# Optimization experiments

Measured on AMD Instinct MI355X. Metric: run time of the kernel, lower is better.

## Reference

```python
import jax, jax.numpy as jnp
import numpy as np
from jax import lax


def conv2d(x, w, b=None, pad=0):
    y = lax.conv_general_dilated(x, w, (1, 1), [(pad, pad), (pad, pad)],
                                 dimension_numbers=('NCHW', 'OIHW', 'NCHW'))
    if b is not None:
        y = y + b[None, :, None, None]
    return y


def setup_inputs():
    key = jax.random.key(0)
    ks = jax.random.split(key, 8)
    B, C, H, W = 8, 3, 224, 224
    OC, NH, HD = 32, 8, 4
    s = lambda fan: 1.0 / np.sqrt(fan)
    x = jax.random.normal(ks[0], (B, C, H, W), jnp.float32)
    # gumbel noise for the hard gumbel-softmax over attention logits [B,NH,HD,H,H]
    gumbel = jax.random.gumbel(ks[1], (B, NH, HD, H, H), jnp.float32)
    in_w = jax.random.normal(ks[2], (OC, C, 3, 3), jnp.float32) * s(C * 9)
    in_b = jnp.zeros((OC,), jnp.float32)
    qkv_w = jax.random.normal(ks[3], (3 * OC, OC, 3, 3), jnp.float32) * s(OC * 9)
    proj_w = jax.random.normal(ks[4], (OC, OC, 1, 1), jnp.float32) * s(OC)
    proj_b = jnp.zeros((OC,), jnp.float32)
    upd_w = jax.random.normal(ks[5], (OC, OC, 1, 1), jnp.float32) * s(OC)
    upd_b = jnp.zeros((OC,), jnp.float32)
    bn_gamma = jnp.ones((OC,), jnp.float32)
    bn_beta = jnp.zeros((OC,), jnp.float32)
    return {"x": x, "gumbel": gumbel, "in_w": in_w, "in_b": in_b, "qkv_w": qkv_w,
            "proj_w": proj_w, "proj_b": proj_b, "upd_w": upd_w, "upd_b": upd_b,
            "bn_gamma": bn_gamma, "bn_beta": bn_beta}


def reference(x, gumbel, in_w, in_b, qkv_w, proj_w, proj_b, upd_w, upd_b, bn_gamma, bn_beta):
    B, _, H, W = x.shape
    NH, HD = 8, 4
    OC = NH * HD
    EPS = 1e-5
    x1 = conv2d(x, in_w, in_b, pad=1)                       # [B,32,H,W]
    qkv = conv2d(x1, qkv_w, None, pad=1).reshape(B, NH, 3, HD, H, W)
    q, k, v = qkv[:, :, 0], qkv[:, :, 1], qkv[:, :, 2]      # each [B,NH,HD,H,W]
    scale = HD ** -0.5
    # matmul(q, k^T) over the last two dims -> [B,NH,HD,H,H]
    logits = jnp.einsum('bndiw,bndjw->bndij', q, k) * scale
    # hard gumbel-softmax, tau=1, straight-through
    y_soft = jax.nn.softmax(logits + gumbel, axis=-1)
    idx = jnp.argmax(y_soft, axis=-1)
    y_hard = jax.nn.one_hot(idx, H, dtype=y_soft.dtype)
    att = y_hard - lax.stop_gradient(y_soft) + y_soft
    A = jnp.einsum('bndij,bndjw->bndiw', att, v).reshape(B, OC, H, W)
    # F.interpolate to (224,224) bilinear is identity since H=W=224
    A = conv2d(A, proj_w, proj_b)
    A = conv2d(A, upd_w, upd_b)
    # BatchNorm2d in training mode (batch statistics, biased variance)
    mean = A.mean(axis=(0, 2, 3), keepdims=True)
    var = ((A - mean) ** 2).mean(axis=(0, 2, 3), keepdims=True)
    A = (A - mean) * lax.rsqrt(var + EPS)
    A = A * bn_gamma[None, :, None, None] + bn_beta[None, :, None, None]
    A = A * jax.nn.sigmoid(A)  # SiLU; dropout is identity (eval)
    out = A + x1
    return out, att
```

## Files before the change

### kernel.cpp

```cpp
#include <hip/hip_runtime.h>
#include <hip/hip_bf16.h>

#define NB 8
#define CIN 3
#define HH 224
#define WW 224
#define OC 32
#define NH 8
#define HD 4
#define NHD 32
#define C96 96
#define HWSZ (HH*WW)

#define HT 4
#define OCT 8
#define NGB 4

__global__ void k_w2(const float* __restrict__ pw, const float* __restrict__ pb,
                     const float* __restrict__ uw, const float* __restrict__ ub,
                     float* __restrict__ W2, float* __restrict__ b2) {
    int c = threadIdx.x, o = threadIdx.y;
    float acc = 0.f;
    for (int m = 0; m < OC; ++m) acc = fmaf(uw[o*OC + m], pw[m*OC + c], acc);
    W2[o*OC + c] = acc;
    if (c == 0) {
        float bb = ub[o];
        for (int m = 0; m < OC; ++m) bb = fmaf(uw[o*OC + m], pb[m], bb);
        b2[o] = bb;
    }
}

__global__ __launch_bounds__(256) void k_conv_in_tile(const float* __restrict__ x,
                                                      const float* __restrict__ w,
                                                      const float* __restrict__ bias,
                                                      float* __restrict__ x1) {
    int h0 = blockIdx.x * 2;
    int b  = blockIdx.y;
    __shared__ float xs[CIN][4][226];
    int t = threadIdx.x;
    for (int ch = 0; ch < CIN; ++ch)
        for (int r = 0; r < 4; ++r) {
            int gh = h0 - 1 + r;
            for (int col = t; col < 226; col += 256) {
                float v = 0.f;
                if (gh >= 0 && gh < HH && col > 0 && col < 225)
                    v = x[((size_t)(b*CIN + ch)*HH + gh)*WW + (col-1)];
                xs[ch][r][col] = v;
            }
        }
    __syncthreads();
    int wv = t;
    if (wv >= WW) return;
    float xv[CIN][4][3];
    #pragma unroll
    for (int c = 0; c < CIN; ++c)
        #pragma unroll
        for (int r = 0; r < 4; ++r)
            #pragma unroll
            for (int j = 0; j < 3; ++j)
                xv[c][r][j] = xs[c][r][wv + j];
    float acc[2][OC];
    #pragma unroll
    for (int hy = 0; hy < 2; ++hy)
        for (int oc = 0; oc < OC; ++oc) acc[hy][oc] = 0.f;
    #pragma unroll
    for (int c = 0; c < CIN; ++c)
        #pragma unroll
        for (int kh = 0; kh < 3; ++kh)
            #pragma unroll
            for (int kw = 0; kw < 3; ++kw)
                for (int oc = 0; oc < OC; ++oc) {
                    float wgt = w[oc*CIN*9 + c*9 + kh*3 + kw];
                    #pragma unroll
                    for (int hy = 0; hy < 2; ++hy)
                        acc[hy][oc] = fmaf(xv[c][hy+kh][kw], wgt, acc[hy][oc]);
                }
    for (int oc = 0; oc < OC; ++oc) {
        float bs = bias[oc];
        #pragma unroll
        for (int hy = 0; hy < 2; ++hy)
            x1[((size_t)(b*OC + oc)*HH + (h0+hy))*WW + wv] = __fadd_rn(acc[hy][oc], bs);
    }
}

__global__ __launch_bounds__(256) void k_conv_qkv_tile(const float* __restrict__ x1g,
                                                       const float* __restrict__ w,
                                                       float* __restrict__ qk4,
                                                       float* __restrict__ vbg) {
    int h0 = blockIdx.x * HT;
    int og = blockIdx.y * OCT;
    int z  = blockIdx.z;
    const float* x1b = x1g + (size_t)z*OC*HWSZ;
    float* qk = qk4 + (size_t)z*64*HWSZ;
    float* vb = vbg + (size_t)z*OC*HWSZ;
    __shared__ float xs[2][HT+2][226];
    int t = threadIdx.x;
    int wv = t;
    float acc[HT][OCT];
    #pragma unroll
    for (int a = 0; a < HT; ++a)
        #pragma unroll
        for (int o = 0; o < OCT; ++o) acc[a][o] = 0.f;

    for (int r = 0; r < HT+2; ++r) {
        int gh = h0 - 1 + r;
        for (int col = t; col < 226; col += 256) {
            float v = 0.f;
            if (gh >= 0 && gh < HH && col > 0 && col < 225)
                v = x1b[((size_t)0*HH + gh)*WW + (col-1)];
            xs[0][r][col] = v;
        }
    }
    __syncthreads();

    for (int c = 0; c < OC; ++c) {
        int cur = c & 1;
        if (c + 1 < OC) {
            int nxt = cur ^ 1;
            for (int r = 0; r < HT+2; ++r) {
                int gh = h0 - 1 + r;
                for (int col = t; col < 226; col += 256) {
                    float v = 0.f;
                    if (gh >= 0 && gh < HH && col > 0 && col < 225)
                        v = x1b[((size_t)(c+1)*HH + gh)*WW + (col-1)];
                    xs[nxt][r][col] = v;
                }
            }
        }
        if (wv < WW) {
            float xv[HT+2][3];
            #pragma unroll
            for (int r = 0; r < HT+2; ++r)
                #pragma unroll
                for (int j = 0; j < 3; ++j)
                    xv[r][j] = xs[cur][r][wv + j];
            #pragma unroll
            for (int o = 0; o < OCT; ++o) {
                const float* wr = w + ((size_t)(og + o)*OC + c)*9;
                #pragma unroll
                for (int kh = 0; kh < 3; ++kh)
                    #pragma unroll
                    for (int kw = 0; kw < 3; ++kw) {
                        float wgt = wr[kh*3 + kw];
                        #pragma unroll
                        for (int hy = 0; hy < HT; ++hy)
                            acc[hy][o] = fmaf(xv[hy+kh][kw], wgt, acc[hy][o]);
                    }
            }
        }
        __syncthreads();
    }
    if (wv < WW) {
        #pragma unroll
        for (int o = 0; o < OCT; ++o) {
            int oc = og + o;
            int n = oc / 12, rem = oc % 12;
            int r = rem >> 2, d = rem & 3;
            #pragma unroll
            for (int hy = 0; hy < HT; ++hy) {
                int h = h0 + hy;
                if (r < 2)
                    qk[((size_t)(n*8 + r*4 + d)*HH + h)*WW + wv] = acc[hy][o];
                else
                    vb[((size_t)(n*4 + d)*HH + h)*WW + wv] = acc[hy][o];
            }
        }
    }
}

__global__ __launch_bounds__(256) void k_attn_ri(const float* __restrict__ qk,
                                                 const float* __restrict__ gum,
                                                 float* __restrict__ att,
                                                 int* __restrict__ idxout) {
    int i0 = blockIdx.x * 8;
    int nd = blockIdx.y;
    int n = nd >> 2, d = nd & 3;
    const float* qb = qk + ((size_t)(n*8 + d)*HH + i0)*WW;
    const float* kb = qk + ((size_t)(n*8 + 4 + d)*HH)*WW;
    __shared__ __align__(16) float qs[8][WW];
    __shared__ float vals[8][256];
    __shared__ int   win_s[8];
    int t = threadIdx.x;
    for (int f = t; f < 8*(WW/4); f += 256) {
        int r = f / (WW/4), p = (f % (WW/4))*4;
        *(float4*)(&qs[r][p]) = *(const float4*)(qb + (size_t)r*WW + p);
    }
    __syncthreads();
    if (t < WW) {
        const float* kr = kb + (size_t)t*WW;
        float s0[8], s1[8], s2[8], s3[8];
        #pragma unroll
        for (int ii = 0; ii < 8; ++ii) { s0[ii]=0.f; s1[ii]=0.f; s2[ii]=0.f; s3[ii]=0.f; }
        for (int w = 0; w < WW; w += 4) {
            float4 kc = *(const float4*)(kr + w);
            #pragma unroll
            for (int ii = 0; ii < 8; ++ii) {
                float4 qc = *(const float4*)(&qs[ii][w]);
                s0[ii] = __fadd_rn(s0[ii], __fmul_rn(qc.x, kc.x));
                s1[ii] = __fadd_rn(s1[ii], __fmul_rn(qc.y, kc.y));
                s2[ii] = __fadd_rn(s2[ii], __fmul_rn(qc.z, kc.z));
                s3[ii] = __fadd_rn(s3[ii], __fmul_rn(qc.w, kc.w));
            }
        }
        #pragma unroll
        for (int ii = 0; ii < 8; ++ii) {
            float dot = __fadd_rn(__fadd_rn(s0[ii], s1[ii]), __fadd_rn(s2[ii], s3[ii]));
            vals[ii][t] = __fadd_rn(__fmul_rn(0.5f, dot),
                                    gum[((size_t)nd*HH + (i0 + ii))*HH + t]);
        }
    } else {
        #pragma unroll
        for (int ii = 0; ii < 8; ++ii) vals[ii][t] = -INFINITY;
    }
    __syncthreads();
    int ii = t >> 5, jj = t & 31;
    float best = -INFINITY; int bj = 0x7fffffff;
    for (int j = jj; j < 256; j += 32) {
        float v = vals[ii][j];
        if (v > best) { best = v; bj = j; }
    }
    for (int off = 16; off > 0; off >>= 1) {
        float v2 = __shfl_down(best, off, 32);
        int   j2 = __shfl_down(bj,   off, 32);
        if (v2 > best || (v2 == best && j2 < bj)) { best = v2; bj = j2; }
    }
    if (jj == 0) { win_s[ii] = bj; idxout[nd*HH + i0 + ii] = bj; }
    __syncthreads();
    for (int e = t; e < 8*WW; e += 256) {
        int r = e / WW, j = e - r*WW;
        att[((size_t)nd*HH + (i0 + r))*HH + j] = (j == win_s[r]) ? 1.f : 0.f;
    }
}

__global__ void k_gather_mm(const float* __restrict__ vbuf,
                            const int* __restrict__ idx,
                            const float* __restrict__ W2g,
                            const float* __restrict__ b2g,
                            float* __restrict__ A2) {
    int i = blockIdx.x, b = blockIdx.y;
    __shared__ float w2s[OC*OC];
    __shared__ float b2s[OC];
    __shared__ int   id[OC];
    for (int t = threadIdx.x; t < OC*OC; t += blockDim.x) w2s[t] = W2g[t];
    if (threadIdx.x < OC) {
        b2s[threadIdx.x] = b2g[threadIdx.x];
        id[threadIdx.x]  = idx[(b*NHD + threadIdx.x)*HH + i];
    }
    __syncthreads();
    int wv = threadIdx.x;
    if (wv >= WW) return;
    float vals[OC];
    for (int c = 0; c < OC; ++c)
        vals[c] = vbuf[((size_t)(b*OC + c)*HH + id[c])*WW + wv];
    for (int oc = 0; oc < OC; ++oc) {
        float a = b2s[oc];
        for (int c = 0; c < OC; ++c) a = fmaf(w2s[oc*OC + c], vals[c], a);
        A2[((size_t)(b*OC + oc)*HH + i)*WW + wv] = a;
    }
}

__global__ __launch_bounds__(256) void k_stats(const float* __restrict__ A2,
                                               float* __restrict__ sums,
                                               float* __restrict__ sumsq) {
    int oc = blockIdx.x, s = blockIdx.y;
    int t = threadIdx.x;
    float a = 0.f, a2 = 0.f;
    const int SL = HWSZ/16;
    for (int b = 0; b < NB; ++b) {
        const float* base = A2 + (size_t)(b*OC + oc)*HWSZ + s*SL;
        for (int e = t*4; e < SL; e += 256*4) {
            float4 v = *(const float4*)(base + e);
            a  += v.x + v.y + v.z + v.w;
            a2 += v.x*v.x + v.y*v.y + v.z*v.z + v.w*v.w;
        }
    }
    __shared__ float r1[256], r2[256];
    r1[t] = a; r2[t] = a2;
    __syncthreads();
    for (int st = 128; st > 0; st >>= 1) {
        if (t < st) { r1[t] += r1[t+st]; r2[t] += r2[t+st]; }
        __syncthreads();
    }
    if (t == 0) { atomicAdd(&sums[oc], r1[0]); atomicAdd(&sumsq[oc], r2[0]); }
}

__global__ __launch_bounds__(256) void k_final(const float* __restrict__ A2,
                                               const float* __restrict__ x1,
                                               const float* __restrict__ sums,
                                               const float* __restrict__ sumsq,
                                               const float* __restrict__ gamma,
                                               const float* __restrict__ beta,
                                               float* __restrict__ out) {
    int i = blockIdx.x, b = blockIdx.y;
    __shared__ float mean_s[OC], inv_s[OC], g_s[OC], be_s[OC];
    if (threadIdx.x < OC) {
        int oc = threadIdx.x;
        const float N = (float)(NB*HH*WW);
        float mean = sums[oc]/N;
        float var  = sumsq[oc]/N - mean*mean;
        mean_s[oc] = mean;
        inv_s[oc]  = rsqrtf(var + 1e-5f);
        g_s[oc]    = gamma[oc];
        be_s[oc]   = beta[oc];
    }
    __syncthreads();
    int wv = threadIdx.x;
    if (wv >= WW) return;
    for (int oc = 0; oc < OC; ++oc) {
        size_t o = ((size_t)(b*OC + oc)*HH + i)*WW + wv;
        float a = A2[o];
        float an = (a - mean_s[oc])*inv_s[oc]*g_s[oc] + be_s[oc];
        float sw = an / (1.f + __expf(-an));
        out[o] = sw + x1[o];
    }
}

extern "C" void kernel_launch(void* const* d_in, const int* in_sizes, int n_in,
                              void* d_out, int out_size, void* d_ws, size_t ws_size,
                              hipStream_t stream) {
    const float* x      = (const float*)d_in[0];
    const float* gumbel = (const float*)d_in[1];
    const float* in_w   = (const float*)d_in[2];
    const float* in_b   = (const float*)d_in[3];
    const float* qkv_w  = (const float*)d_in[4];
    const float* proj_w = (const float*)d_in[5];
    const float* proj_b = (const float*)d_in[6];
    const float* upd_w  = (const float*)d_in[7];
    const float* upd_b  = (const float*)d_in[8];
    const float* bng    = (const float*)d_in[9];
    const float* bnb    = (const float*)d_in[10];

    float* out = (float*)d_out;
    float* att = out + (size_t)NB*OC*HWSZ;

    float* x1   = (float*)d_ws;
    float* qk4  = x1 + (size_t)NB*OC*HWSZ;
    float* A2   = qk4;
    float* vbuf = qk4 + (size_t)NGB*64*HWSZ;
    float* W2   = vbuf + (size_t)NB*OC*HWSZ;
    float* b2   = W2 + OC*OC;
    float* sums = b2 + OC;
    float* sumsq= sums + OC;
    int*   idx  = (int*)(sumsq + OC);

    hipMemsetAsync(sums, 0, 2*OC*sizeof(float), stream);

    k_w2          <<<1, dim3(OC, OC), 0, stream>>>(proj_w, proj_b, upd_w, upd_b, W2, b2);
    k_conv_in_tile<<<dim3(HH/2, NB), 256, 0, stream>>>(x, in_w, in_b, x1);

    for (int g = 0; g < NB/NGB; ++g) {
        k_conv_qkv_tile<<<dim3(HH/HT, C96/OCT, NGB), 256, 0, stream>>>(
            x1 + (size_t)g*NGB*OC*HWSZ, qkv_w, qk4, vbuf + (size_t)g*NGB*OC*HWSZ);
        for (int z = 0; z < NGB; ++z) {
            int b = g*NGB + z;
            k_attn_ri<<<dim3(HH/8, NHD), 256, 0, stream>>>(
                qk4    + (size_t)z*64*HWSZ,
                gumbel + (size_t)b*NH*HD*HH*HH,
                att    + (size_t)b*NH*HD*HH*HH,
                idx    + (size_t)b*NHD*HH);
        }
    }

    k_gather_mm<<<dim3(HH, NB), 256, 0, stream>>>(vbuf, idx, W2, b2, A2);
    k_stats    <<<dim3(OC, 16), 256, 0, stream>>>(A2, sums, sumsq);
    k_final    <<<dim3(HH, NB), 256, 0, stream>>>(A2, x1, sums, sumsq, bng, bnb, out);
}
```

Baseline: 881.8 us.

## Pad x1 buffer for vectorized halo loads, regroup qkv conv per head, batch attention launches

x1 is now stored in a zero-padded 226x228 layout, and a memset clears its border. The qkv conv can then copy halo rows with unguarded float4 loads instead of branchy scalar loads. The conv block now computes all 12 channels of one head (OCT 12), which simplifies the output index math but raises register pressure. The four per-batch attention launches are merged into one launch with a z grid dimension, at the cost of an extra full-buffer memset and a larger workspace.

```diff
diff --git a/kernel.cpp b/kernel.cpp
--- a/kernel.cpp
+++ b/kernel.cpp
@@ -12,8 +12,12 @@
 #define C96 96
 #define HWSZ (HH*WW)
 
+#define PH 226
+#define PW 228
+#define CHS (PH*PW)
+
 #define HT 4
-#define OCT 8
+#define OCT 12
 #define NGB 4
 
 __global__ void k_w2(const float* __restrict__ pw, const float* __restrict__ pb,
@@ -79,7 +83,7 @@
         float bs = bias[oc];
         #pragma unroll
         for (int hy = 0; hy < 2; ++hy)
-            x1[((size_t)(b*OC + oc)*HH + (h0+hy))*WW + wv] = __fadd_rn(acc[hy][oc], bs);
+            x1[((size_t)(b*OC + oc)*PH + (h0+hy+1))*PW + (wv+1)] = __fadd_rn(acc[hy][oc], bs);
     }
 }
 
@@ -88,44 +92,34 @@
                                                        float* __restrict__ qk4,
                                                        float* __restrict__ vbg) {
     int h0 = blockIdx.x * HT;
-    int og = blockIdx.y * OCT;
+    int n  = blockIdx.y;
     int z  = blockIdx.z;
-    const float* x1b = x1g + (size_t)z*OC*HWSZ;
+    const float* x1b = x1g + (size_t)z*OC*CHS;
     float* qk = qk4 + (size_t)z*64*HWSZ;
     float* vb = vbg + (size_t)z*OC*HWSZ;
-    __shared__ float xs[2][HT+2][226];
+    __shared__ float xs[2][(HT+2)*PW];
     int t = threadIdx.x;
     int wv = t;
+    int og = n * OCT;
     float acc[HT][OCT];
     #pragma unroll
     for (int a = 0; a < HT; ++a)
         #pragma unroll
         for (int o = 0; o < OCT; ++o) acc[a][o] = 0.f;
 
-    for (int r = 0; r < HT+2; ++r) {
-        int gh = h0 - 1 + r;
-        for (int col = t; col < 226; col += 256) {
-            float v = 0.f;
-            if (gh >= 0 && gh < HH && col > 0 && col < 225)
-                v = x1b[((size_t)0*HH + gh)*WW + (col-1)];
-            xs[0][r][col] = v;
-        }
+    {
+        const float4* s = (const float4*)(x1b + (size_t)h0*PW);
+        float4* d = (float4*)xs[0];
+        for (int f = t; f < (HT+2)*PW/4; f += 256) d[f] = s[f];
     }
     __syncthreads();
 
     for (int c = 0; c < OC; ++c) {
         int cur = c & 1;
         if (c + 1 < OC) {
-            int nxt = cur ^ 1;
-            for (int r = 0; r < HT+2; ++r) {
-                int gh = h0 - 1 + r;
-                for (int col = t; col < 226; col += 256) {
-                    float v = 0.f;
-                    if (gh >= 0 && gh < HH && col > 0 && col < 225)
-                        v = x1b[((size_t)(c+1)*HH + gh)*WW + (col-1)];
-                    xs[nxt][r][col] = v;
-                }
-            }
+            const float4* s = (const float4*)(x1b + (size_t)(c+1)*CHS + (size_t)h0*PW);
+            float4* d = (float4*)xs[cur ^ 1];
+            for (int f = t; f < (HT+2)*PW/4; f += 256) d[f] = s[f];
         }
         if (wv < WW) {
             float xv[HT+2][3];
@@ -133,7 +127,7 @@
             for (int r = 0; r < HT+2; ++r)
                 #pragma unroll
                 for (int j = 0; j < 3; ++j)
-                    xv[r][j] = xs[cur][r][wv + j];
+                    xv[r][j] = xs[cur][r*PW + wv + j];
             #pragma unroll
             for (int o = 0; o < OCT; ++o) {
                 const float* wr = w + ((size_t)(og + o)*OC + c)*9;
@@ -153,9 +147,7 @@
     if (wv < WW) {
         #pragma unroll
         for (int o = 0; o < OCT; ++o) {
-            int oc = og + o;
-            int n = oc / 12, rem = oc % 12;
-            int r = rem >> 2, d = rem & 3;
+            int r = o >> 2, d = o & 3;
             #pragma unroll
             for (int hy = 0; hy < HT; ++hy) {
                 int h = h0 + hy;
@@ -168,15 +160,22 @@
     }
 }
 
-__global__ __launch_bounds__(256) void k_attn_ri(const float* __restrict__ qk,
+__global__ __launch_bounds__(256) void k_attn_ri(const float* __restrict__ qk4,
                                                  const float* __restrict__ gum,
                                                  float* __restrict__ att,
-                                                 int* __restrict__ idxout) {
+                                                 int* __restrict__ idxout,
+                                                 int b0) {
     int i0 = blockIdx.x * 8;
     int nd = blockIdx.y;
+    int z  = blockIdx.z;
+    int b  = b0 + z;
+    const float* qkz = qk4 + (size_t)z*64*HWSZ;
+    const float* gumb = gum + (size_t)b*NHD*HH*HH;
+    float* attb = att + (size_t)b*NHD*HH*HH;
+    int* idxb = idxout + (size_t)b*NHD*HH;
     int n = nd >> 2, d = nd & 3;
-    const float* qb = qk + ((size_t)(n*8 + d)*HH + i0)*WW;
-    const float* kb = qk + ((size_t)(n*8 + 4 + d)*HH)*WW;
+    const float* qb = qkz + ((size_t)(n*8 + d)*HH + i0)*WW;
+    const float* kb = qkz + ((size_t)(n*8 + 4 + d)*HH)*WW;
     __shared__ __align__(16) float qs[8][WW];
     __shared__ float vals[8][256];
     __shared__ int   win_s[8];
@@ -206,7 +205,7 @@
         for (int ii = 0; ii < 8; ++ii) {
             float dot = __fadd_rn(__fadd_rn(s0[ii], s1[ii]), __fadd_rn(s2[ii], s3[ii]));
             vals[ii][t] = __fadd_rn(__fmul_rn(0.5f, dot),
-                                    gum[((size_t)nd*HH + (i0 + ii))*HH + t]);
+                                    gumb[((size_t)nd*HH + (i0 + ii))*HH + t]);
         }
     } else {
         #pragma unroll
@@ -224,11 +223,11 @@
         int   j2 = __shfl_down(bj,   off, 32);
         if (v2 > best || (v2 == best && j2 < bj)) { best = v2; bj = j2; }
     }
-    if (jj == 0) { win_s[ii] = bj; idxout[nd*HH + i0 + ii] = bj; }
+    if (jj == 0) { win_s[ii] = bj; idxb[nd*HH + i0 + ii] = bj; }
     __syncthreads();
     for (int e = t; e < 8*WW; e += 256) {
         int r = e / WW, j = e - r*WW;
-        att[((size_t)nd*HH + (i0 + r))*HH + j] = (j == win_s[r]) ? 1.f : 0.f;
+        attb[((size_t)nd*HH + (i0 + r))*HH + j] = (j == win_s[r]) ? 1.f : 0.f;
     }
 }
 
@@ -311,7 +310,7 @@
         float a = A2[o];
         float an = (a - mean_s[oc])*inv_s[oc]*g_s[oc] + be_s[oc];
         float sw = an / (1.f + __expf(-an));
-        out[o] = sw + x1[o];
+        out[o] = sw + x1[((size_t)(b*OC + oc)*PH + (i+1))*PW + (wv+1)];
     }
 }
 
@@ -334,7 +333,7 @@
     float* att = out + (size_t)NB*OC*HWSZ;
 
     float* x1   = (float*)d_ws;
-    float* qk4  = x1 + (size_t)NB*OC*HWSZ;
+    float* qk4  = x1 + (size_t)NB*OC*CHS;
     float* A2   = qk4;
     float* vbuf = qk4 + (size_t)NGB*64*HWSZ;
     float* W2   = vbuf + (size_t)NB*OC*HWSZ;
@@ -343,6 +342,7 @@
     float* sumsq= sums + OC;
     int*   idx  = (int*)(sumsq + OC);
 
+    hipMemsetAsync(x1, 0, (size_t)NB*OC*CHS*sizeof(float), stream);
     hipMemsetAsync(sums, 0, 2*OC*sizeof(float), stream);
 
     k_w2          <<<1, dim3(OC, OC), 0, stream>>>(proj_w, proj_b, upd_w, upd_b, W2, b2);
@@ -350,15 +350,9 @@
 
     for (int g = 0; g < NB/NGB; ++g) {
         k_conv_qkv_tile<<<dim3(HH/HT, C96/OCT, NGB), 256, 0, stream>>>(
-            x1 + (size_t)g*NGB*OC*HWSZ, qkv_w, qk4, vbuf + (size_t)g*NGB*OC*HWSZ);
-        for (int z = 0; z < NGB; ++z) {
-            int b = g*NGB + z;
-            k_attn_ri<<<dim3(HH/8, NHD), 256, 0, stream>>>(
-                qk4    + (size_t)z*64*HWSZ,
-                gumbel + (size_t)b*NH*HD*HH*HH,
-                att    + (size_t)b*NH*HD*HH*HH,
-                idx    + (size_t)b*NHD*HH);
-        }
+            x1 + (size_t)g*NGB*OC*CHS, qkv_w, qk4, vbuf + (size_t)g*NGB*OC*HWSZ);
+        k_attn_ri<<<dim3(HH/8, NHD, NGB), 256, 0, stream>>>(
+            qk4, gumbel, att, idx, g*NGB);
     }
 
     k_gather_mm<<<dim3(HH, NB), 256, 0, stream>>>(vbuf, idx, W2, b2, A2);
```

Result: slower. 963.2 us (+9.2%).
